# Kernel tuning notes

Measured on AMD Instinct MI355X. Metric: run time of the kernel, lower is better.

The kernel has to match this reference:

```python
import jax, jax.numpy as jnp
import numpy as np

BS, NUM_PATCH, N_VARS, PATCH_LEN, D_MODEL = 32, 64, 321, 12, 128
TIME_RATIO, FREQ_RATIO = 0.5, 0.4


def setup_inputs() -> dict:
    key = jax.random.key(0)
    ks = jax.random.split(key, 7)
    x = jax.random.normal(ks[0], (BS, NUM_PATCH, N_VARS, PATCH_LEN), jnp.float32)
    W_in = jax.random.normal(ks[1], (PATCH_LEN, D_MODEL), jnp.float32) / np.sqrt(PATCH_LEN)
    b_in = jnp.zeros((D_MODEL,), jnp.float32)
    W_out = jax.random.normal(ks[2], (D_MODEL, PATCH_LEN), jnp.float32) / np.sqrt(D_MODEL)
    b_out = jnp.zeros((PATCH_LEN,), jnp.float32)
    # nn.Parameter(torch.zeros(1,1,1)) in the original; use small random scalars so grads are non-trivial
    time_mask_token = jax.random.normal(ks[3], (), jnp.float32) * 0.02
    freq_mask_token = jax.random.normal(ks[4], (), jnp.float32) * 0.02
    return {"x": x, "W_in": W_in, "b_in": b_in, "W_out": W_out, "b_out": b_out,
            "time_mask_token": time_mask_token, "freq_mask_token": freq_mask_token}


def _scatter_mask(idx, num_patch):
    # idx: [bs, n_vars, k] patch indices to mask (set False). Returns bool [bs, num_patch, n_vars].
    bs, nv, k = idx.shape
    m = jnp.ones((bs, num_patch, nv), dtype=bool)
    b = jnp.arange(bs)[:, None, None]
    v = jnp.arange(nv)[None, :, None]
    return m.at[b, idx, v].set(False)


def reference(x, W_in, b_in, W_out, b_out, time_mask_token, freq_mask_token):
    bs, num_patch, n_vars, patch_len = x.shape

    # patch2emb applied per token (equivalent to the gather-encode path since the
    # projection is pointwise per patch): [bs, np, nv, d_model]
    emb = jnp.einsum('bpvl,ld->bpvd', x, W_in) + b_in

    # ---- time masking: mask patches with highest coefficient of variation ----
    cv = jnp.std(x, axis=-1, ddof=1) / (jnp.mean(x, axis=-1) + 1e-6)  # [bs, np, nv]
    k_t = int(num_patch * TIME_RATIO)
    _, idx_t = jax.lax.top_k(jnp.transpose(cv, (0, 2, 1)), k_t)       # [bs, nv, k_t]
    mask_t = _scatter_mask(idx_t, num_patch)                           # True = keep
    tokens_t = jnp.where(mask_t[..., None], emb, time_mask_token)
    out_t = jnp.einsum('bpvd,dl->bpvl', tokens_t, W_out) + b_out

    # ---- freq masking: mask patches with lowest mean FFT magnitude ----
    mag = jnp.abs(jnp.fft.rfft(x, axis=-1))                            # [bs, np, nv, pl//2+1]
    score = mag.mean(axis=-1)                                          # [bs, np, nv]
    k_f = int(num_patch * FREQ_RATIO)
    _, idx_f = jax.lax.top_k(-jnp.transpose(score, (0, 2, 1)), k_f)    # smallest scores
    mask_f = _scatter_mask(idx_f, num_patch)
    tokens_f = jnp.where(mask_f[..., None], emb, freq_mask_token)
    out_f = jnp.einsum('bpvd,dl->bpvl', tokens_f, W_out) + b_out

    return out_t * 0.5 + out_f * 0.5
```

## Files before the change

kernel.cpp:

```cpp
#include <hip/hip_runtime.h>
#include <math.h>

constexpr int BS = 32, NV = 321, PL = 12, DM = 128;
constexpr int KT = 32;
constexpr int KF = 25;
constexpr int VB = 4;
constexpr int NCHUNK = 81;
constexpr int SST = 72;

__global__ void prep_kernel(const float* __restrict__ W_in,
                            const float* __restrict__ b_in,
                            const float* __restrict__ W_out,
                            const float* __restrict__ b_out,
                            const float* __restrict__ tt,
                            const float* __restrict__ ft,
                            float* __restrict__ prep) {
  int t = threadIdx.x;
  if (t < 144) {
    int i = t / 12, l = t % 12;
    const float4* Wi = (const float4*)(W_in + i * DM);
    float s = 0.f;
#pragma unroll 8
    for (int d4 = 0; d4 < 32; ++d4) {
      float4 a = Wi[d4];
      const float* wo = W_out + d4 * 48 + l;
      s += a.x * wo[0] + a.y * wo[12] + a.z * wo[24] + a.w * wo[36];
    }
    prep[t] = s;
  } else if (t < 168) {
    int l = (t - 144) % 12;
    float cs = 0.f, cb = 0.f;
#pragma unroll 8
    for (int d = 0; d < DM; ++d) {
      float w = W_out[d * 12 + l];
      cs += w;
      cb += b_in[d] * w;
    }
    if (t < 156) {
      prep[144 + l] = cb;
      prep[156 + l] = tt[0] * cs;
    } else {
      prep[168 + l] = ft[0] * cs;
    }
  } else if (t < 180) {
    prep[180 + (t - 168)] = b_out[t - 168];
  }
}

__global__ __launch_bounds__(256) void fused_kernel(
    const float* __restrict__ x, const float* __restrict__ prep,
    float* __restrict__ out) {
  __shared__ float scv[VB * SST];
  __shared__ float sfs[VB * SST];

  const int t = threadIdx.x;
  const int chunk = blockIdx.x;
  const int b = blockIdx.y;
  const int v0 = chunk * VB;
  const bool full = (chunk < 80);
  const int p = t >> 2;
  const int vv = t & 3;
  const bool valid = full || (vv == 0);

  float xr[12];
  if (valid) {
    const float4* src =
        (const float4*)(x + (((size_t)(b * 64 + p) * NV) + v0 + vv) * PL);
    float4 a = src[0], bb = src[1], c = src[2];
    xr[0] = a.x;  xr[1] = a.y;  xr[2] = a.z;  xr[3] = a.w;
    xr[4] = bb.x; xr[5] = bb.y; xr[6] = bb.z; xr[7] = bb.w;
    xr[8] = c.x;  xr[9] = c.y;  xr[10] = c.z; xr[11] = c.w;
  }

  float cv = 0.f, fs = 0.f;
  const float H = 0.86602540378443864676f;
  if (valid) {
    const float* xv = xr;
    float s = 0.f;
#pragma unroll
    for (int i = 0; i < 12; ++i) s += xv[i];
    const float m = s * (1.0f / 12.0f);
    float ss = 0.f;
#pragma unroll
    for (int i = 0; i < 12; ++i) {
      float d = xv[i] - m;
      ss += d * d;
    }
    cv = sqrtf(ss * (1.0f / 11.0f)) / (m + 1e-6f);

    const float e1 = xv[1] + xv[11], e2 = xv[2] + xv[10], e3 = xv[3] + xv[9],
                e4 = xv[4] + xv[8], e5 = xv[5] + xv[7];
    const float o1 = xv[1] - xv[11], o2 = xv[2] - xv[10], o3 = xv[3] - xv[9],
                o4 = xv[4] - xv[8], o5 = xv[5] - xv[7];
    float mag = fabsf(xv[0] + xv[6] + e1 + e2 + e3 + e4 + e5);
    float re = xv[0] - xv[6] + H * (e1 - e5) + 0.5f * (e2 - e4);
    float im = 0.5f * (o1 + o5) + H * (o2 + o4) + o3;
    mag += sqrtf(re * re + im * im);
    re = xv[0] + xv[6] + 0.5f * (e1 + e5) - 0.5f * (e2 + e4) - e3;
    im = H * (o1 + o2 - o4 - o5);
    mag += sqrtf(re * re + im * im);
    re = xv[0] - xv[6] - e2 + e4;
    im = o1 - o3 + o5;
    mag += sqrtf(re * re + im * im);
    re = xv[0] + xv[6] - 0.5f * (e1 + e2 + e4 + e5) + e3;
    im = H * (o1 - o2 + o4 - o5);
    mag += sqrtf(re * re + im * im);
    re = xv[0] - xv[6] + H * (e5 - e1) + 0.5f * (e2 - e4);
    im = 0.5f * (o1 + o5) - H * (o2 + o4) + o3;
    mag += sqrtf(re * re + im * im);
    re = xv[0] + xv[6] - e1 + e2 - e3 + e4 - e5;
    mag += fabsf(re);
    fs = mag * (1.0f / 7.0f);

    scv[vv * SST + p] = cv;
    sfs[vv * SST + p] = fs;
  }
  __syncthreads();

  int gt_t = 0, eqb_t = 0, gt_f = 0, eqb_f = 0;
  if (valid) {
    const float4* rc = (const float4*)(scv + vv * SST);
    const float4* rf = (const float4*)(sfs + vv * SST);
#pragma unroll
    for (int q4 = 0; q4 < 16; ++q4) {
      const float4 c4 = rc[q4];
      const float4 f4 = rf[q4];
      const int q = q4 * 4;
      gt_t += (c4.x > cv) + (c4.y > cv) + (c4.z > cv) + (c4.w > cv);
      gt_f += (f4.x < fs) + (f4.y < fs) + (f4.z < fs) + (f4.w < fs);
      eqb_t += ((c4.x == cv) & (q + 0 < p)) + ((c4.y == cv) & (q + 1 < p)) +
               ((c4.z == cv) & (q + 2 < p)) + ((c4.w == cv) & (q + 3 < p));
      eqb_f += ((f4.x == fs) & (q + 0 < p)) + ((f4.y == fs) & (q + 1 < p)) +
               ((f4.z == fs) & (q + 2 < p)) + ((f4.w == fs) & (q + 3 < p));
    }
  }
  const bool kt = (gt_t + eqb_t) >= KT;
  const bool kf = (gt_f + eqb_f) >= KF;

  float E[12];
#pragma unroll
  for (int l = 0; l < 12; ++l) E[l] = prep[144 + l];
#pragma unroll
  for (int i = 0; i < 12; ++i) {
    const float a = xr[i];
#pragma unroll
    for (int l = 0; l < 12; ++l) E[l] += a * prep[i * 12 + l];
  }
  if (valid) {
    float o[12];
#pragma unroll
    for (int l = 0; l < 12; ++l) {
      const float at = kt ? E[l] : prep[156 + l];
      const float af = kf ? E[l] : prep[168 + l];
      o[l] = 0.5f * (at + af) + prep[180 + l];
    }
    float* op = out + (((size_t)(b * 64 + p) * NV) + v0 + vv) * PL;
    ((float4*)op)[0] = make_float4(o[0], o[1], o[2], o[3]);
    ((float4*)op)[1] = make_float4(o[4], o[5], o[6], o[7]);
    ((float4*)op)[2] = make_float4(o[8], o[9], o[10], o[11]);
  }
}

extern "C" void kernel_launch(void* const* d_in, const int* in_sizes, int n_in,
                              void* d_out, int out_size, void* d_ws,
                              size_t ws_size, hipStream_t stream) {
  const float* x = (const float*)d_in[0];
  const float* W_in = (const float*)d_in[1];
  const float* b_in = (const float*)d_in[2];
  const float* W_out = (const float*)d_in[3];
  const float* b_out = (const float*)d_in[4];
  const float* tt = (const float*)d_in[5];
  const float* ft = (const float*)d_in[6];
  float* out = (float*)d_out;
  float* prep = (float*)d_ws;

  hipLaunchKernelGGL(prep_kernel, dim3(1), dim3(192), 0, stream, W_in, b_in,
                     W_out, b_out, tt, ft, prep);
  hipLaunchKernelGGL(fused_kernel, dim3(NCHUNK, BS), dim3(256), 0, stream, x,
                     prep, out);
}
```

Baseline: 130.3 us.

## Fuse weight precompute into main kernel and use ballot radix-select for top-k

Removes the separate single-block prep kernel. Each block now recomputes the 12x12 folded weight matrix and the bias and mask-token terms into shared memory. The O(64) per-thread rank counting is replaced by a wavefront ballot-based bitwise radix select on order-preserving unsigned keys, with ties broken by lane index. The mask bits are published through shared memory after an extra barrier. The trade-off is redundant weight work (about 4K FMAs over 144 threads) in every one of the 2592 blocks, in exchange for saving a kernel launch and its serialization.

```diff
diff --git a/kernel.cpp b/kernel.cpp
--- a/kernel.cpp
+++ b/kernel.cpp
@@ -8,50 +8,20 @@
 constexpr int NCHUNK = 81;
 constexpr int SST = 72;
 
-__global__ void prep_kernel(const float* __restrict__ W_in,
-                            const float* __restrict__ b_in,
-                            const float* __restrict__ W_out,
-                            const float* __restrict__ b_out,
-                            const float* __restrict__ tt,
-                            const float* __restrict__ ft,
-                            float* __restrict__ prep) {
-  int t = threadIdx.x;
-  if (t < 144) {
-    int i = t / 12, l = t % 12;
-    const float4* Wi = (const float4*)(W_in + i * DM);
-    float s = 0.f;
-#pragma unroll 8
-    for (int d4 = 0; d4 < 32; ++d4) {
-      float4 a = Wi[d4];
-      const float* wo = W_out + d4 * 48 + l;
-      s += a.x * wo[0] + a.y * wo[12] + a.z * wo[24] + a.w * wo[36];
-    }
-    prep[t] = s;
-  } else if (t < 168) {
-    int l = (t - 144) % 12;
-    float cs = 0.f, cb = 0.f;
-#pragma unroll 8
-    for (int d = 0; d < DM; ++d) {
-      float w = W_out[d * 12 + l];
-      cs += w;
-      cb += b_in[d] * w;
-    }
-    if (t < 156) {
-      prep[144 + l] = cb;
-      prep[156 + l] = tt[0] * cs;
-    } else {
-      prep[168 + l] = ft[0] * cs;
-    }
-  } else if (t < 180) {
-    prep[180 + (t - 168)] = b_out[t - 168];
-  }
+__device__ __forceinline__ unsigned ord(float f) {
+  unsigned u = __float_as_uint(f);
+  return ((int)u < 0) ? ~u : (u | 0x80000000u);
 }
 
 __global__ __launch_bounds__(256) void fused_kernel(
-    const float* __restrict__ x, const float* __restrict__ prep,
-    float* __restrict__ out) {
+    const float* __restrict__ x, const float* __restrict__ W_in,
+    const float* __restrict__ b_in, const float* __restrict__ W_out,
+    const float* __restrict__ b_out, const float* __restrict__ tt,
+    const float* __restrict__ ft, float* __restrict__ out) {
   __shared__ float scv[VB * SST];
   __shared__ float sfs[VB * SST];
+  __shared__ __align__(16) float spp[192];
+  __shared__ unsigned long long smT[VB], smF[VB];
 
   const int t = threadIdx.x;
   const int chunk = blockIdx.x;
@@ -72,7 +42,36 @@
     xr[8] = c.x;  xr[9] = c.y;  xr[10] = c.z; xr[11] = c.w;
   }
 
-  float cv = 0.f, fs = 0.f;
+  if (t < 144) {
+    const int i = t / 12, l = t - (t / 12) * 12;
+    const float4* Wi = (const float4*)(W_in + i * DM);
+    float s = 0.f;
+#pragma unroll 8
+    for (int d4 = 0; d4 < 32; ++d4) {
+      float4 a = Wi[d4];
+      const float* wo = W_out + d4 * 48 + l;
+      s += a.x * wo[0] + a.y * wo[12] + a.z * wo[24] + a.w * wo[36];
+    }
+    spp[t] = s;
+  } else if (t < 168) {
+    const int l = (t - 144) % 12;
+    float cs = 0.f, cb = 0.f;
+#pragma unroll 8
+    for (int d = 0; d < DM; ++d) {
+      float w = W_out[d * 12 + l];
+      cs += w;
+      cb += b_in[d] * w;
+    }
+    if (t < 156) {
+      spp[144 + l] = cb;
+      spp[156 + l] = tt[0] * cs;
+    } else {
+      spp[168 + l] = ft[0] * cs;
+    }
+  } else if (t < 180) {
+    spp[180 + (t - 168)] = b_out[t - 168];
+  }
+
   const float H = 0.86602540378443864676f;
   if (valid) {
     const float* xv = xr;
@@ -86,7 +85,7 @@
       float d = xv[i] - m;
       ss += d * d;
     }
-    cv = sqrtf(ss * (1.0f / 11.0f)) / (m + 1e-6f);
+    const float cv = sqrtf(ss * (1.0f / 11.0f)) / (m + 1e-6f);
 
     const float e1 = xv[1] + xv[11], e2 = xv[2] + xv[10], e3 = xv[3] + xv[9],
                 e4 = xv[4] + xv[8], e5 = xv[5] + xv[7];
@@ -110,49 +109,64 @@
     mag += sqrtf(re * re + im * im);
     re = xv[0] + xv[6] - e1 + e2 - e3 + e4 - e5;
     mag += fabsf(re);
-    fs = mag * (1.0f / 7.0f);
+    const float fs = mag * (1.0f / 7.0f);
 
     scv[vv * SST + p] = cv;
     sfs[vv * SST + p] = fs;
   }
   __syncthreads();
 
-  int gt_t = 0, eqb_t = 0, gt_f = 0, eqb_f = 0;
-  if (valid) {
-    const float4* rc = (const float4*)(scv + vv * SST);
-    const float4* rf = (const float4*)(sfs + vv * SST);
+  const int wv = t >> 6, lane = t & 63;
+  if (full || wv == 0) {
+    const unsigned ut = ord(scv[wv * SST + lane]);
+    const unsigned uf = ~ord(sfs[wv * SST + lane]);
+    unsigned tht = 0, thf = 0;
 #pragma unroll
-    for (int q4 = 0; q4 < 16; ++q4) {
-      const float4 c4 = rc[q4];
-      const float4 f4 = rf[q4];
-      const int q = q4 * 4;
-      gt_t += (c4.x > cv) + (c4.y > cv) + (c4.z > cv) + (c4.w > cv);
-      gt_f += (f4.x < fs) + (f4.y < fs) + (f4.z < fs) + (f4.w < fs);
-      eqb_t += ((c4.x == cv) & (q + 0 < p)) + ((c4.y == cv) & (q + 1 < p)) +
-               ((c4.z == cv) & (q + 2 < p)) + ((c4.w == cv) & (q + 3 < p));
-      eqb_f += ((f4.x == fs) & (q + 0 < p)) + ((f4.y == fs) & (q + 1 < p)) +
-               ((f4.z == fs) & (q + 2 < p)) + ((f4.w == fs) & (q + 3 < p));
+    for (int bit = 31; bit >= 0; --bit) {
+      const unsigned ct = tht | (1u << bit);
+      const unsigned cf = thf | (1u << bit);
+      const unsigned long long bt = __ballot(ut >= ct);
+      const unsigned long long bf = __ballot(uf >= cf);
+      if (__popcll(bt) >= KT) tht = ct;
+      if (__popcll(bf) >= KF) thf = cf;
+    }
+    const unsigned long long pre = (1ull << lane) - 1ull;
+    const int gt_t = __popcll(__ballot(ut > tht));
+    const int rt = __popcll(__ballot(ut == tht) & pre);
+    const bool masked_t = (ut > tht) || ((ut == tht) && (rt < KT - gt_t));
+    const int gt_f = __popcll(__ballot(uf > thf));
+    const int rf = __popcll(__ballot(uf == thf) & pre);
+    const bool masked_f = (uf > thf) || ((uf == thf) && (rf < KF - gt_f));
+    const unsigned long long bkt = __ballot(!masked_t);
+    const unsigned long long bkf = __ballot(!masked_f);
+    if (lane == 0) {
+      smT[wv] = bkt;
+      smF[wv] = bkf;
     }
   }
-  const bool kt = (gt_t + eqb_t) >= KT;
-  const bool kf = (gt_f + eqb_f) >= KF;
+  __syncthreads();
 
+  const bool kt = (smT[vv] >> p) & 1ull;
+  const bool kf = (smF[vv] >> p) & 1ull;
   float E[12];
 #pragma unroll
-  for (int l = 0; l < 12; ++l) E[l] = prep[144 + l];
+  for (int l = 0; l < 12; ++l) E[l] = spp[144 + l];
+  const float4* M4 = (const float4*)spp;
 #pragma unroll
   for (int i = 0; i < 12; ++i) {
+    const float4 m0 = M4[i * 3], m1 = M4[i * 3 + 1], m2 = M4[i * 3 + 2];
     const float a = xr[i];
-#pragma unroll
-    for (int l = 0; l < 12; ++l) E[l] += a * prep[i * 12 + l];
+    E[0] += a * m0.x;  E[1] += a * m0.y;  E[2] += a * m0.z;  E[3] += a * m0.w;
+    E[4] += a * m1.x;  E[5] += a * m1.y;  E[6] += a * m1.z;  E[7] += a * m1.w;
+    E[8] += a * m2.x;  E[9] += a * m2.y;  E[10] += a * m2.z; E[11] += a * m2.w;
   }
   if (valid) {
     float o[12];
 #pragma unroll
     for (int l = 0; l < 12; ++l) {
-      const float at = kt ? E[l] : prep[156 + l];
-      const float af = kf ? E[l] : prep[168 + l];
-      o[l] = 0.5f * (at + af) + prep[180 + l];
+      const float at = kt ? E[l] : spp[156 + l];
+      const float af = kf ? E[l] : spp[168 + l];
+      o[l] = 0.5f * (at + af) + spp[180 + l];
     }
     float* op = out + (((size_t)(b * 64 + p) * NV) + v0 + vv) * PL;
     ((float4*)op)[0] = make_float4(o[0], o[1], o[2], o[3]);
@@ -172,10 +186,7 @@
   const float* tt = (const float*)d_in[5];
   const float* ft = (const float*)d_in[6];
   float* out = (float*)d_out;
-  float* prep = (float*)d_ws;
 
-  hipLaunchKernelGGL(prep_kernel, dim3(1), dim3(192), 0, stream, W_in, b_in,
-                     W_out, b_out, tt, ft, prep);
   hipLaunchKernelGGL(fused_kernel, dim3(NCHUNK, BS), dim3(256), 0, stream, x,
-                     prep, out);
+                     W_in, b_in, W_out, b_out, tt, ft, out);
 }
```

After: 122.6 us. 5.9% less time.
